# Performance work log

Hardware: AMD Instinct MI355X
Metric: run time of the kernel (lower is better)

Reference implementation:

```python
import jax, jax.numpy as jnp
import numpy as np

N, H, E = 40000, 128, 640000
BN_EPS = 1e-5


def setup_inputs() -> dict:
    key = jax.random.key(0)
    ks = jax.random.split(key, 5)
    x = jax.random.normal(ks[0], (N, H), dtype=jnp.float32)
    edge_index = jax.random.randint(ks[1], (2, E), 0, N, dtype=jnp.int64)
    eps = jnp.zeros((1,), dtype=jnp.float32)
    s = 1.0 / np.sqrt(H)  # torch Linear init scale
    W1 = jax.random.uniform(ks[2], (H, H), jnp.float32, -s, s)
    b1 = jnp.zeros((H,), dtype=jnp.float32)
    W2 = jax.random.uniform(ks[3], (H, H), jnp.float32, -s, s)
    b2 = jnp.zeros((H,), dtype=jnp.float32)
    gamma = jnp.ones((H,), dtype=jnp.float32)
    beta = jnp.zeros((H,), dtype=jnp.float32)
    return {"x": x, "edge_index": edge_index, "eps": eps,
            "W1": W1, "b1": b1, "W2": W2, "b2": b2,
            "gamma": gamma, "beta": beta}


def reference(x, edge_index, eps, W1, b1, W2, b2, gamma, beta):
    src = edge_index[0]
    tgt = edge_index[1]
    # gather source features, scatter-add into target rows: [N, H]
    agg = jax.ops.segment_sum(x[src], tgt, num_segments=x.shape[0])
    out = agg + (1.0 + eps) * x
    # MLP: Linear -> ReLU -> Linear -> BatchNorm1d (train mode) -> ReLU
    h = jax.nn.relu(out @ W1.T + b1)
    h = h @ W2.T + b2
    mean = jnp.mean(h, axis=0)
    var = jnp.mean((h - mean) ** 2, axis=0)  # biased var, as BN uses
    h = (h - mean) * jax.lax.rsqrt(var + BN_EPS) * gamma + beta
    return jax.nn.relu(h)
```

## Files before the change

kernel.cpp:

```cpp
#include <hip/hip_runtime.h>

#define HDIM 128
#define BN_EPS 1e-5f
#define SCAN_BINS 1024
#define LSTR 136
#define MROWS 16
#define NREP 8

typedef short short8 __attribute__((ext_vector_type(8)));
typedef float floatx4 __attribute__((ext_vector_type(4)));

__device__ __forceinline__ unsigned short f2b(float f) {
    union { float f; unsigned u; } v; v.f = f;
    unsigned r = v.u + 0x7FFFu + ((v.u >> 16) & 1u);
    return (unsigned short)(r >> 16);
}

__device__ __forceinline__ float b2f(unsigned short b) {
    union { unsigned u; float f; } v; v.u = (unsigned)b << 16;
    return v.f;
}

__global__ __launch_bounds__(256) void prep_kernel(
    const float* __restrict__ x, unsigned short* __restrict__ xB, long n4,
    const float* __restrict__ W1, const float* __restrict__ W2,
    unsigned short* __restrict__ W1B, unsigned short* __restrict__ W2B,
    const int* __restrict__ eidx, int* __restrict__ hist,
    int* __restrict__ rank, float* __restrict__ statSum, int E, int N)
{
    int tid = blockIdx.x * 256 + threadIdx.x;
    int stride = gridDim.x * 256;
    if (blockIdx.x == 0 && threadIdx.x < 32) {
        ushort4 z; z.x = 0; z.y = 0; z.z = 0; z.w = 0;
        ((ushort4*)(xB + (size_t)N * HDIM))[threadIdx.x] = z;
    }
    if (blockIdx.x == 1) {
        for (int i = threadIdx.x; i < 2 * NREP * HDIM; i += 256)
            statSum[i] = 0.f;
    }
    for (long i = tid; i < n4; i += stride) {
        float4 v = ((const float4*)x)[i];
        ushort4 o;
        o.x = f2b(v.x); o.y = f2b(v.y); o.z = f2b(v.z); o.w = f2b(v.w);
        ((ushort4*)xB)[i] = o;
    }
    for (int i = tid; i < HDIM * HDIM; i += stride) {
        W1B[i] = f2b(W1[i]);
        W2B[i] = f2b(W2[i]);
    }
    int E4 = E >> 2;
    const int4* tgt4 = (const int4*)(eidx + E);
    for (int e4 = tid; e4 < E4; e4 += stride) {
        int4 t = tgt4[e4];
        int4 r;
        r.x = atomicAdd(&hist[t.x], 1);
        r.y = atomicAdd(&hist[t.y], 1);
        r.z = atomicAdd(&hist[t.z], 1);
        r.w = atomicAdd(&hist[t.w], 1);
        ((int4*)rank)[e4] = r;
    }
    for (int e = E4 * 4 + tid; e < E; e += stride) {
        rank[e] = atomicAdd(&hist[eidx[E + e]], 1);
    }
}

__global__ __launch_bounds__(256) void scan_fused_kernel(
    const int* __restrict__ hist, int* __restrict__ offsets,
    int* __restrict__ blockSums, int* __restrict__ spin,
    int* __restrict__ srcSorted, int N, int NB)
{
    __shared__ int ts[256];
    __shared__ int bs[64];
    __shared__ int sPr;
    int b = blockIdx.x, t = threadIdx.x;
    int base = b * SCAN_BINS + t * 4;
    int4 h = make_int4(0, 0, 0, 0);
    if (base + 3 < N) {
        h = *(const int4*)(hist + base);
    } else {
        if (base + 0 < N) h.x = hist[base + 0];
        if (base + 1 < N) h.y = hist[base + 1];
        if (base + 2 < N) h.z = hist[base + 2];
    }
    int4 p;
    p.x = (h.x + 7) & ~7;
    p.y = (h.y + 7) & ~7;
    p.z = (h.z + 7) & ~7;
    p.w = (h.w + 7) & ~7;
    int s = p.x + p.y + p.z + p.w;
    ts[t] = s;
    __syncthreads();
    for (int off = 1; off < 256; off <<= 1) {
        int v = ts[t];
        int add = (t >= off) ? ts[t - off] : 0;
        __syncthreads();
        ts[t] = v + add;
        __syncthreads();
    }
    int excl = ts[t] - s;
    if (t == 0) {
        blockSums[b] = ts[255];
        __threadfence();
        atomicAdd(spin, 1);
        while (__hip_atomic_load(spin, __ATOMIC_ACQUIRE,
                                 __HIP_MEMORY_SCOPE_AGENT) < NB) {
            __builtin_amdgcn_s_sleep(8);
        }
    }
    __syncthreads();
    if (t < NB) bs[t] = blockSums[t];
    __syncthreads();
    if (t == 0) {
        int pr = 0;
        for (int i = 0; i < b; i++) pr += bs[i];
        sPr = pr;
        if (b == 0) {
            int tot = 0;
            for (int i = 0; i < NB; i++) tot += bs[i];
            offsets[N] = tot;
        }
    }
    __syncthreads();
    int prefix = sPr;
    int4 o;
    o.x = prefix + excl;
    o.y = o.x + p.x;
    o.z = o.y + p.y;
    o.w = o.z + p.z;
    if (base + 3 < N) {
        *(int4*)(offsets + base) = o;
    } else {
        if (base + 0 < N) offsets[base + 0] = o.x;
        if (base + 1 < N) offsets[base + 1] = o.y;
        if (base + 2 < N) offsets[base + 2] = o.z;
    }
    for (int q = o.x + h.x; q < o.x + p.x; q++) srcSorted[q] = N;
    for (int q = o.y + h.y; q < o.y + p.y; q++) srcSorted[q] = N;
    for (int q = o.z + h.z; q < o.z + p.z; q++) srcSorted[q] = N;
    for (int q = o.w + h.w; q < o.w + p.w; q++) srcSorted[q] = N;
}

__global__ __launch_bounds__(256) void reorder_kernel(
    const int* __restrict__ eidx, const int* __restrict__ offsets,
    const int* __restrict__ rank, int* __restrict__ srcSorted, int E)
{
    int stride = gridDim.x * 256;
    for (int e = blockIdx.x * 256 + threadIdx.x; e < E; e += stride) {
        int t = eidx[E + e];
        srcSorted[offsets[t] + rank[e]] = eidx[e];
    }
}

__global__ __launch_bounds__(256, 8) void mega_kernel(
    const unsigned short* __restrict__ xB,
    const int* __restrict__ offsets, const int* __restrict__ srcSorted,
    const float* __restrict__ eps,
    const unsigned short* __restrict__ W1B, const float* __restrict__ b1,
    const unsigned short* __restrict__ W2B, const float* __restrict__ b2,
    float* __restrict__ out, float* __restrict__ statSum,
    float* __restrict__ statSqs, int N)
{
    __shared__ unsigned short sA[MROWS * LSTR];
    __shared__ unsigned short sH[MROWS * LSTR];

    int tid = threadIdx.x;
    int rb = blockIdx.x * MROWS;

    float coef = 1.0f + eps[0];
    int tx = tid & 15, ty = tid >> 4;
    int col = tx * 8;
    {
        int row = rb + ty;
        float acc[8] = {0.f, 0.f, 0.f, 0.f, 0.f, 0.f, 0.f, 0.f};
        if (row < N) {
            short8 xv = *(const short8*)(xB + (size_t)row * HDIM + col);
            #pragma unroll
            for (int j = 0; j < 8; j++) acc[j] = coef * b2f((unsigned short)xv[j]);
            int beg = offsets[row];
            int nb = (offsets[row + 1] - beg) >> 3;
            const int4* sp = (const int4*)(srcSorted + beg);
            int4 ia, ib;
            if (nb > 0) { ia = sp[0]; ib = sp[1]; }
            for (int b = 0; b < nb; b++) {
                short8 u[8];
                u[0] = *(const short8*)(xB + (size_t)ia.x * HDIM + col);
                u[1] = *(const short8*)(xB + (size_t)ia.y * HDIM + col);
                u[2] = *(const short8*)(xB + (size_t)ia.z * HDIM + col);
                u[3] = *(const short8*)(xB + (size_t)ia.w * HDIM + col);
                u[4] = *(const short8*)(xB + (size_t)ib.x * HDIM + col);
                u[5] = *(const short8*)(xB + (size_t)ib.y * HDIM + col);
                u[6] = *(const short8*)(xB + (size_t)ib.z * HDIM + col);
                u[7] = *(const short8*)(xB + (size_t)ib.w * HDIM + col);
                sp += 2;
                if (b + 1 < nb) { ia = sp[0]; ib = sp[1]; }
                #pragma unroll
                for (int q = 0; q < 8; q++)
                    #pragma unroll
                    for (int j = 0; j < 8; j++)
                        acc[j] += b2f((unsigned short)u[q][j]);
            }
        }
        short8 o;
        #pragma unroll
        for (int j = 0; j < 8; j++) o[j] = (short)f2b(acc[j]);
        *(short8*)(sA + ty * LSTR + col) = o;
    }
    __syncthreads();

    int w = tid >> 6;
    int l = tid & 63;
    int m = l & 15, quad = l >> 4;
    int cbase = w * 32;

    floatx4 acc1[2];
    #pragma unroll
    for (int t = 0; t < 2; t++) acc1[t] = (floatx4){0.f, 0.f, 0.f, 0.f};
    #pragma unroll
    for (int kk = 0; kk < 4; kk++) {
        int k0 = kk * 32 + quad * 8;
        short8 a = *(const short8*)(sA + m * LSTR + k0);
        #pragma unroll
        for (int t = 0; t < 2; t++) {
            short8 bfr = *(const short8*)(W1B + (size_t)(cbase + t * 16 + m) * HDIM + k0);
            acc1[t] = __builtin_amdgcn_mfma_f32_16x16x32_bf16(a, bfr, acc1[t], 0, 0, 0);
        }
    }
    #pragma unroll
    for (int t = 0; t < 2; t++) {
        int colc = cbase + t * 16 + m;
        float bs = b1[colc];
        #pragma unroll
        for (int r = 0; r < 4; r++) {
            float v = fmaxf(acc1[t][r] + bs, 0.f);
            sH[(quad * 4 + r) * LSTR + colc] = f2b(v);
        }
    }
    __syncthreads();

    floatx4 acc2[2];
    #pragma unroll
    for (int t = 0; t < 2; t++) acc2[t] = (floatx4){0.f, 0.f, 0.f, 0.f};
    #pragma unroll
    for (int kk = 0; kk < 4; kk++) {
        int k0 = kk * 32 + quad * 8;
        short8 a = *(const short8*)(sH + m * LSTR + k0);
        #pragma unroll
        for (int t = 0; t < 2; t++) {
            short8 bfr = *(const short8*)(W2B + (size_t)(cbase + t * 16 + m) * HDIM + k0);
            acc2[t] = __builtin_amdgcn_mfma_f32_16x16x32_bf16(a, bfr, acc2[t], 0, 0, 0);
        }
    }
    float* repSum = statSum + (blockIdx.x & (NREP - 1)) * HDIM;
    float* repSqs = statSqs + (blockIdx.x & (NREP - 1)) * HDIM;
    int row0 = rb + quad * 4;
    #pragma unroll
    for (int t = 0; t < 2; t++) {
        int colc = cbase + t * 16 + m;
        float bs = b2[colc];
        float cs = 0.f, cq = 0.f;
        #pragma unroll
        for (int r = 0; r < 4; r++) {
            int row = row0 + r;
            if (row < N) {
                float v = acc2[t][r] + bs;
                out[(size_t)row * HDIM + colc] = v;
                cs += v; cq += v * v;
            }
        }
        cs += __shfl_xor(cs, 16, 64);
        cs += __shfl_xor(cs, 32, 64);
        cq += __shfl_xor(cq, 16, 64);
        cq += __shfl_xor(cq, 32, 64);
        if (quad == 0) {
            atomicAdd(&repSum[colc], cs);
            atomicAdd(&repSqs[colc], cq);
        }
    }
}

__global__ __launch_bounds__(256) void bn_apply_kernel(
    float* __restrict__ out, const float* __restrict__ statSum,
    const float* __restrict__ statSqs, const float* __restrict__ gamma,
    const float* __restrict__ beta, int N, long n4)
{
    __shared__ float sSc[HDIM];
    __shared__ float sSh[HDIM];
    int t = threadIdx.x;
    if (t < HDIM) {
        float s = 0.f, q = 0.f;
        #pragma unroll
        for (int r = 0; r < NREP; r++) {
            s += statSum[r * HDIM + t];
            q += statSqs[r * HDIM + t];
        }
        float invN = 1.0f / (float)N;
        float mean = s * invN;
        float var = q * invN - mean * mean;
        float sc = gamma[t] * rsqrtf(var + BN_EPS);
        sSc[t] = sc;
        sSh[t] = beta[t] - mean * sc;
    }
    __syncthreads();
    long stride = (long)gridDim.x * 256;
    for (long i = (long)blockIdx.x * 256 + t; i < n4; i += stride) {
        int cg = (int)(i & 31) * 4;
        float4 v = ((float4*)out)[i];
        v.x = fmaxf(v.x * sSc[cg + 0] + sSh[cg + 0], 0.f);
        v.y = fmaxf(v.y * sSc[cg + 1] + sSh[cg + 1], 0.f);
        v.z = fmaxf(v.z * sSc[cg + 2] + sSh[cg + 2], 0.f);
        v.w = fmaxf(v.w * sSc[cg + 3] + sSh[cg + 3], 0.f);
        ((float4*)out)[i] = v;
    }
}

extern "C" void kernel_launch(void* const* d_in, const int* in_sizes, int n_in,
                              void* d_out, int out_size, void* d_ws, size_t ws_size,
                              hipStream_t stream) {
    const float* x     = (const float*)d_in[0];
    const int*   eidx  = (const int*)d_in[1];
    const float* eps   = (const float*)d_in[2];
    const float* W1    = (const float*)d_in[3];
    const float* b1    = (const float*)d_in[4];
    const float* W2    = (const float*)d_in[5];
    const float* b2    = (const float*)d_in[6];
    const float* gamma = (const float*)d_in[7];
    const float* beta  = (const float*)d_in[8];
    float* out = (float*)d_out;

    int N = in_sizes[0] / HDIM;
    int E = in_sizes[1] / 2;
    size_t NH = (size_t)N * HDIM;
    int NB = (N + SCAN_BINS - 1) / SCAN_BINS;
    int NpadOff = (N + 1 + 3) & ~3;
    long n4 = (long)NH / 4;
    int Emax = E + 7 * N + 64;

    unsigned short* xB   = (unsigned short*)d_ws;
    unsigned short* W1B  = xB + NH + HDIM;
    unsigned short* W2B  = W1B + HDIM * HDIM;
    float* statSum = (float*)(W2B + HDIM * HDIM);
    float* statSqs = statSum + NREP * HDIM;
    int*   hist    = (int*)(statSqs + NREP * HDIM);
    int*   spin    = hist + N;
    int*   offsets = spin + 16;
    int*   rank    = offsets + NpadOff;
    int*   srcSorted = rank + E;
    int*   blockSums = srcSorted + Emax;

    hipMemsetAsync(hist, 0, (size_t)(N + 16) * sizeof(int), stream);
    prep_kernel<<<1280, 256, 0, stream>>>(x, xB, n4, W1, W2, W1B, W2B,
                                          eidx, hist, rank, statSum, E, N);
    scan_fused_kernel<<<NB, 256, 0, stream>>>(hist, offsets, blockSums,
                                              spin, srcSorted, N, NB);
    reorder_kernel<<<1024, 256, 0, stream>>>(eidx, offsets, rank, srcSorted, E);
    int gblocks = (N + MROWS - 1) / MROWS;
    mega_kernel<<<gblocks, 256, 0, stream>>>(
        xB, offsets, srcSorted, eps, W1B, b1, W2B, b2,
        out, statSum, statSqs, N);
    bn_apply_kernel<<<2048, 256, 0, stream>>>(
        out, statSum, statSqs, gamma, beta, N, n4);
}
```

Measured before the change: 174.3 us.

## Fuse scan with reorder via grid barrier and store pre-BN activations in bf16

Merges the scan and reorder kernels into one launch of 512 blocks. The first NB blocks do the prefix scan, then every block waits on a global spin counter before scattering edges into sorted order. The mega kernel now writes the pre-BatchNorm output as bf16 into a workspace buffer, and bn_apply reads it and writes the fp32 result, which halves the intermediate write and read traffic. The risks are lower precision in the pre-BN values and a grid-wide spin barrier that assumes all 512 blocks are resident at the same time.

```diff
diff --git a/kernel.cpp b/kernel.cpp
--- a/kernel.cpp
+++ b/kernel.cpp
@@ -6,6 +6,7 @@
 #define LSTR 136
 #define MROWS 16
 #define NREP 8
+#define RGRID 512
 
 typedef short short8 __attribute__((ext_vector_type(8)));
 typedef float floatx4 __attribute__((ext_vector_type(4)));
@@ -64,90 +65,102 @@
     }
 }
 
-__global__ __launch_bounds__(256) void scan_fused_kernel(
+__global__ __launch_bounds__(256) void scanreorder_kernel(
     const int* __restrict__ hist, int* __restrict__ offsets,
     int* __restrict__ blockSums, int* __restrict__ spin,
-    int* __restrict__ srcSorted, int N, int NB)
+    int* __restrict__ srcSorted, const int* __restrict__ eidx,
+    const int* __restrict__ rank, int E, int N, int NB)
 {
     __shared__ int ts[256];
     __shared__ int bs[64];
     __shared__ int sPr;
     int b = blockIdx.x, t = threadIdx.x;
-    int base = b * SCAN_BINS + t * 4;
-    int4 h = make_int4(0, 0, 0, 0);
-    if (base + 3 < N) {
-        h = *(const int4*)(hist + base);
-    } else {
-        if (base + 0 < N) h.x = hist[base + 0];
-        if (base + 1 < N) h.y = hist[base + 1];
-        if (base + 2 < N) h.z = hist[base + 2];
-    }
-    int4 p;
-    p.x = (h.x + 7) & ~7;
-    p.y = (h.y + 7) & ~7;
-    p.z = (h.z + 7) & ~7;
-    p.w = (h.w + 7) & ~7;
-    int s = p.x + p.y + p.z + p.w;
-    ts[t] = s;
+
+    if (b < NB) {
+        int base = b * SCAN_BINS + t * 4;
+        int4 h = make_int4(0, 0, 0, 0);
+        if (base + 3 < N) {
+            h = *(const int4*)(hist + base);
+        } else {
+            if (base + 0 < N) h.x = hist[base + 0];
+            if (base + 1 < N) h.y = hist[base + 1];
+            if (base + 2 < N) h.z = hist[base + 2];
+        }
+        int4 p;
+        p.x = (h.x + 7) & ~7;
+        p.y = (h.y + 7) & ~7;
+        p.z = (h.z + 7) & ~7;
+        p.w = (h.w + 7) & ~7;
+        int s = p.x + p.y + p.z + p.w;
+        ts[t] = s;
+        __syncthreads();
+        for (int off = 1; off < 256; off <<= 1) {
+            int v = ts[t];
+            int add = (t >= off) ? ts[t - off] : 0;
+            __syncthreads();
+            ts[t] = v + add;
+            __syncthreads();
+        }
+        int excl = ts[t] - s;
+        if (t == 0) {
+            blockSums[b] = ts[255];
+            __threadfence();
+            atomicAdd(&spin[0], 1);
+            while (__hip_atomic_load(&spin[0], __ATOMIC_ACQUIRE,
+                                     __HIP_MEMORY_SCOPE_AGENT) < NB) {
+                __builtin_amdgcn_s_sleep(8);
+            }
+        }
+        __syncthreads();
+        if (t < NB) bs[t] = blockSums[t];
+        __syncthreads();
+        if (t == 0) {
+            int pr = 0;
+            for (int i = 0; i < b; i++) pr += bs[i];
+            sPr = pr;
+            if (b == 0) {
+                int tot = 0;
+                for (int i = 0; i < NB; i++) tot += bs[i];
+                offsets[N] = tot;
+            }
+        }
+        __syncthreads();
+        int prefix = sPr;
+        int4 o;
+        o.x = prefix + excl;
+        o.y = o.x + p.x;
+        o.z = o.y + p.y;
+        o.w = o.z + p.z;
+        if (base + 3 < N) {
+            *(int4*)(offsets + base) = o;
+        } else {
+            if (base + 0 < N) offsets[base + 0] = o.x;
+            if (base + 1 < N) offsets[base + 1] = o.y;
+            if (base + 2 < N) offsets[base + 2] = o.z;
+        }
+        for (int q = o.x + h.x; q < o.x + p.x; q++) srcSorted[q] = N;
+        for (int q = o.y + h.y; q < o.y + p.y; q++) srcSorted[q] = N;
+        for (int q = o.z + h.z; q < o.z + p.z; q++) srcSorted[q] = N;
+        for (int q = o.w + h.w; q < o.w + p.w; q++) srcSorted[q] = N;
+        __syncthreads();
+        if (t == 0) {
+            __threadfence();
+            atomicAdd(&spin[4], 1);
+        }
+    }
+
+    if (t == 0) {
+        while (__hip_atomic_load(&spin[4], __ATOMIC_ACQUIRE,
+                                 __HIP_MEMORY_SCOPE_AGENT) < NB) {
+            __builtin_amdgcn_s_sleep(32);
+        }
+    }
     __syncthreads();
-    for (int off = 1; off < 256; off <<= 1) {
-        int v = ts[t];
-        int add = (t >= off) ? ts[t - off] : 0;
-        __syncthreads();
-        ts[t] = v + add;
-        __syncthreads();
-    }
-    int excl = ts[t] - s;
-    if (t == 0) {
-        blockSums[b] = ts[255];
-        __threadfence();
-        atomicAdd(spin, 1);
-        while (__hip_atomic_load(spin, __ATOMIC_ACQUIRE,
-                                 __HIP_MEMORY_SCOPE_AGENT) < NB) {
-            __builtin_amdgcn_s_sleep(8);
-        }
-    }
-    __syncthreads();
-    if (t < NB) bs[t] = blockSums[t];
-    __syncthreads();
-    if (t == 0) {
-        int pr = 0;
-        for (int i = 0; i < b; i++) pr += bs[i];
-        sPr = pr;
-        if (b == 0) {
-            int tot = 0;
-            for (int i = 0; i < NB; i++) tot += bs[i];
-            offsets[N] = tot;
-        }
-    }
-    __syncthreads();
-    int prefix = sPr;
-    int4 o;
-    o.x = prefix + excl;
-    o.y = o.x + p.x;
-    o.z = o.y + p.y;
-    o.w = o.z + p.z;
-    if (base + 3 < N) {
-        *(int4*)(offsets + base) = o;
-    } else {
-        if (base + 0 < N) offsets[base + 0] = o.x;
-        if (base + 1 < N) offsets[base + 1] = o.y;
-        if (base + 2 < N) offsets[base + 2] = o.z;
-    }
-    for (int q = o.x + h.x; q < o.x + p.x; q++) srcSorted[q] = N;
-    for (int q = o.y + h.y; q < o.y + p.y; q++) srcSorted[q] = N;
-    for (int q = o.z + h.z; q < o.z + p.z; q++) srcSorted[q] = N;
-    for (int q = o.w + h.w; q < o.w + p.w; q++) srcSorted[q] = N;
-}
-
-__global__ __launch_bounds__(256) void reorder_kernel(
-    const int* __restrict__ eidx, const int* __restrict__ offsets,
-    const int* __restrict__ rank, int* __restrict__ srcSorted, int E)
-{
+
     int stride = gridDim.x * 256;
-    for (int e = blockIdx.x * 256 + threadIdx.x; e < E; e += stride) {
-        int t = eidx[E + e];
-        srcSorted[offsets[t] + rank[e]] = eidx[e];
+    for (int e = b * 256 + t; e < E; e += stride) {
+        int tg = eidx[E + e];
+        srcSorted[offsets[tg] + rank[e]] = eidx[e];
     }
 }
 
@@ -157,7 +170,7 @@
     const float* __restrict__ eps,
     const unsigned short* __restrict__ W1B, const float* __restrict__ b1,
     const unsigned short* __restrict__ W2B, const float* __restrict__ b2,
-    float* __restrict__ out, float* __restrict__ statSum,
+    unsigned short* __restrict__ hB, float* __restrict__ statSum,
     float* __restrict__ statSqs, int N)
 {
     __shared__ unsigned short sA[MROWS * LSTR];
@@ -263,7 +276,7 @@
             int row = row0 + r;
             if (row < N) {
                 float v = acc2[t][r] + bs;
-                out[(size_t)row * HDIM + colc] = v;
+                hB[(size_t)row * HDIM + colc] = f2b(v);
                 cs += v; cq += v * v;
             }
         }
@@ -279,9 +292,10 @@
 }
 
 __global__ __launch_bounds__(256) void bn_apply_kernel(
-    float* __restrict__ out, const float* __restrict__ statSum,
-    const float* __restrict__ statSqs, const float* __restrict__ gamma,
-    const float* __restrict__ beta, int N, long n4)
+    const unsigned short* __restrict__ hB, float* __restrict__ out,
+    const float* __restrict__ statSum, const float* __restrict__ statSqs,
+    const float* __restrict__ gamma, const float* __restrict__ beta,
+    int N, long n8)
 {
     __shared__ float sSc[HDIM];
     __shared__ float sSh[HDIM];
@@ -302,14 +316,21 @@
     }
     __syncthreads();
     long stride = (long)gridDim.x * 256;
-    for (long i = (long)blockIdx.x * 256 + t; i < n4; i += stride) {
-        int cg = (int)(i & 31) * 4;
-        float4 v = ((float4*)out)[i];
-        v.x = fmaxf(v.x * sSc[cg + 0] + sSh[cg + 0], 0.f);
-        v.y = fmaxf(v.y * sSc[cg + 1] + sSh[cg + 1], 0.f);
-        v.z = fmaxf(v.z * sSc[cg + 2] + sSh[cg + 2], 0.f);
-        v.w = fmaxf(v.w * sSc[cg + 3] + sSh[cg + 3], 0.f);
-        ((float4*)out)[i] = v;
+    float4* o4 = (float4*)out;
+    for (long i = (long)blockIdx.x * 256 + t; i < n8; i += stride) {
+        int cg = (int)(i & 15) * 8;
+        short8 hv = ((const short8*)hB)[i];
+        float4 a, b;
+        a.x = fmaxf(b2f((unsigned short)hv[0]) * sSc[cg + 0] + sSh[cg + 0], 0.f);
+        a.y = fmaxf(b2f((unsigned short)hv[1]) * sSc[cg + 1] + sSh[cg + 1], 0.f);
+        a.z = fmaxf(b2f((unsigned short)hv[2]) * sSc[cg + 2] + sSh[cg + 2], 0.f);
+        a.w = fmaxf(b2f((unsigned short)hv[3]) * sSc[cg + 3] + sSh[cg + 3], 0.f);
+        b.x = fmaxf(b2f((unsigned short)hv[4]) * sSc[cg + 4] + sSh[cg + 4], 0.f);
+        b.y = fmaxf(b2f((unsigned short)hv[5]) * sSc[cg + 5] + sSh[cg + 5], 0.f);
+        b.z = fmaxf(b2f((unsigned short)hv[6]) * sSc[cg + 6] + sSh[cg + 6], 0.f);
+        b.w = fmaxf(b2f((unsigned short)hv[7]) * sSc[cg + 7] + sSh[cg + 7], 0.f);
+        o4[2 * i]     = a;
+        o4[2 * i + 1] = b;
     }
 }
 
@@ -333,12 +354,14 @@
     int NB = (N + SCAN_BINS - 1) / SCAN_BINS;
     int NpadOff = (N + 1 + 3) & ~3;
     long n4 = (long)NH / 4;
+    long n8 = (long)NH / 8;
     int Emax = E + 7 * N + 64;
 
     unsigned short* xB   = (unsigned short*)d_ws;
     unsigned short* W1B  = xB + NH + HDIM;
     unsigned short* W2B  = W1B + HDIM * HDIM;
-    float* statSum = (float*)(W2B + HDIM * HDIM);
+    unsigned short* hB   = W2B + HDIM * HDIM;
+    float* statSum = (float*)(hB + NH);
     float* statSqs = statSum + NREP * HDIM;
     int*   hist    = (int*)(statSqs + NREP * HDIM);
     int*   spin    = hist + N;
@@ -350,13 +373,12 @@
     hipMemsetAsync(hist, 0, (size_t)(N + 16) * sizeof(int), stream);
     prep_kernel<<<1280, 256, 0, stream>>>(x, xB, n4, W1, W2, W1B, W2B,
                                           eidx, hist, rank, statSum, E, N);
-    scan_fused_kernel<<<NB, 256, 0, stream>>>(hist, offsets, blockSums,
-                                              spin, srcSorted, N, NB);
-    reorder_kernel<<<1024, 256, 0, stream>>>(eidx, offsets, rank, srcSorted, E);
+    scanreorder_kernel<<<RGRID, 256, 0, stream>>>(
+        hist, offsets, blockSums, spin, srcSorted, eidx, rank, E, N, NB);
     int gblocks = (N + MROWS - 1) / MROWS;
     mega_kernel<<<gblocks, 256, 0, stream>>>(
         xB, offsets, srcSorted, eps, W1B, b1, W2B, b2,
-        out, statSum, statSqs, N);
+        hB, statSum, statSqs, N);
     bn_apply_kernel<<<2048, 256, 0, stream>>>(
-        out, statSum, statSqs, gamma, beta, N, n4);
-}
+        hB, out, statSum, statSqs, gamma, beta, N, n8);
+}
```

New measurement: 228.6 us. +31.1%, slower.
